# Performance work log

Hardware: AMD Instinct MI355X
Metric: run time of the kernel (lower is better)

## Reference

```python
import jax, jax.numpy as jnp
import numpy as np

B, L, H = 32, 2048, 512
EPS = 1e-6


def setup_inputs() -> dict:
    key = jax.random.key(0)
    k1, k2 = jax.random.split(key)
    hidden = jax.random.normal(k1, (B, L, H), dtype=jnp.float32)
    # nn.Linear(H, H): weight [H, H], bias [H]; use kaiming-uniform-like scale
    bound = 1.0 / np.sqrt(H)
    W = jax.random.uniform(k2, (H, H), dtype=jnp.float32, minval=-bound, maxval=bound)
    b = jnp.zeros((H,), dtype=jnp.float32)
    return {"hidden": hidden, "W": W, "b": b}


def reference(hidden, W, b):
    Bn, Ln, Hn = hidden.shape

    def step(M, k):
        # k: [B, H]; key == value == hidden[:, t, :]
        v_pred = jnp.einsum("bij,bj->bi", M, k)               # M @ k
        denom = jnp.sum(k * k, axis=-1, keepdims=True) + EPS   # [B, 1]
        delta_v = k - v_pred / denom                           # v - v_pred/denom (v == k)
        M = M + jnp.einsum("bi,bj->bij", delta_v, k)           # outer-product update
        return M, None

    M0 = jnp.zeros((Bn, Hn, Hn), dtype=hidden.dtype)
    xs = jnp.swapaxes(hidden[:, :-1, :], 0, 1)  # [L-1, B, H]
    M, _ = jax.lax.scan(step, M0, xs)

    query = hidden[:, -1, :]                                   # [B, H]
    context = jnp.einsum("bij,bj->bi", M, query)               # [B, H]
    return context @ W.T + b                                   # read_proj
```

## Files before the change

kernel.cpp:

```cpp
#include <hip/hip_runtime.h>
#include <hip/hip_fp16.h>

#define B_  32
#define L_  2048
#define H_  512
#define CA  64
#define NC  32
#define EPSF 1e-6f

typedef _Float16 f16x8 __attribute__((ext_vector_type(8)));
typedef float f32x16 __attribute__((ext_vector_type(16)));

template <int CTRL>
__device__ __forceinline__ float dpp_shift_add(float x) {
  int t = __builtin_amdgcn_update_dpp(0, __float_as_int(x), CTRL, 0xf, 0xf, true);
  return x + __int_as_float(t);
}
__device__ __forceinline__ float wave_reduce_lane63(float x) {
  x = dpp_shift_add<0x111>(x);
  x = dpp_shift_add<0x112>(x);
  x = dpp_shift_add<0x114>(x);
  x = dpp_shift_add<0x118>(x);
  x = dpp_shift_add<0x142>(x);
  x = dpp_shift_add<0x143>(x);
  return x;
}
__device__ __forceinline__ float rdlane(float v, int l) {
  return __int_as_float(__builtin_amdgcn_readlane(__float_as_int(v), l));
}
__device__ __forceinline__ void load_lds16h(const unsigned short* g, unsigned short* l) {
  __builtin_amdgcn_global_load_lds(
      (const __attribute__((address_space(1))) unsigned int*)(g),
      (__attribute__((address_space(3))) unsigned int*)(l), 16, 0, 0);
}

__global__ __launch_bounds__(256) void
deltarule_gram64(const float* __restrict__ hidden,
                 unsigned short* __restrict__ Kh,
                 float* __restrict__ tmT, float* __restrict__ dvec) {
  const int cb = blockIdx.x, b = blockIdx.y;
  const int tid = threadIdx.x, lane = tid & 63, wv = tid >> 6;
  __shared__ __align__(16) unsigned short Kf[CA * H_];
  __shared__ __align__(16) float G[CA * CA];

  const int c0 = cb * CA;
  const float* src = hidden + ((size_t)b * L_ + c0) * H_;
  unsigned short* kout = Kh + ((size_t)b * L_ + c0) * H_;
  const bool lastc = (cb == NC - 1);

#pragma unroll
  for (int u = 0; u < 16; ++u) {
    const int f8 = u * 256 + tid;
    const int row = f8 >> 6;
    const int colf = (f8 & 63) * 8;
    float4 va = *(const float4*)(src + row * H_ + colf);
    float4 vb = *(const float4*)(src + row * H_ + colf + 4);
    if (lastc && row == CA - 1) {
      va = make_float4(0.f, 0.f, 0.f, 0.f);
      vb = make_float4(0.f, 0.f, 0.f, 0.f);
    }
    __half2 h0 = __floats2half2_rn(va.x, va.y);
    __half2 h1 = __floats2half2_rn(va.z, va.w);
    __half2 h2 = __floats2half2_rn(vb.x, vb.y);
    __half2 h3 = __floats2half2_rn(vb.z, vb.w);
    uint4 pk = make_uint4(*(unsigned int*)&h0, *(unsigned int*)&h1,
                          *(unsigned int*)&h2, *(unsigned int*)&h3);
    *(uint4*)&Kf[((colf >> 3) * CA + row) * 8] = pk;
    *(uint4*)(kout + row * H_ + colf) = pk;
  }
  __syncthreads();

  if (wv < 3) {
    const int ta = (wv == 2) ? 1 : 0;
    const int tb = (wv == 0) ? 0 : 1;
    const int mrow = 32 * ta + (lane & 31);
    const int nrow = 32 * tb + (lane & 31);
    const int khi = lane >> 5;
    f32x16 acc;
#pragma unroll
    for (int r = 0; r < 16; ++r) acc[r] = 0.f;
#pragma unroll
    for (int kk = 0; kk < 32; ++kk) {
      const int k8 = 2 * kk + khi;
      const f16x8 av = *(const f16x8*)&Kf[(k8 * CA + mrow) * 8];
      const f16x8 bv = *(const f16x8*)&Kf[(k8 * CA + nrow) * 8];
      acc = __builtin_amdgcn_mfma_f32_32x32x16_f16(av, bv, acc, 0, 0, 0);
    }
#pragma unroll
    for (int r = 0; r < 16; ++r) {
      const int row32 = (r & 3) + 8 * (r >> 2) + 4 * khi;
      G[(32 * ta + row32) * CA + 32 * tb + (lane & 31)] = acc[r];
    }
  }
  __syncthreads();

  if (tid < CA) dvec[((size_t)b * NC + cb) * CA + tid] = G[tid * CA + tid] + EPSF;
  __syncthreads();

  if (wv == 0) {
    const int j = lane & 31;
    float X[32];
#pragma unroll
    for (int t = 31; t >= 0; --t) {
      float i0 = 0.f, i1 = 0.f;
#pragma unroll
      for (int s = t + 1; s < 32; s += 2) i0 = fmaf(G[t * CA + s], X[s], i0);
#pragma unroll
      for (int s = t + 2; s < 32; s += 2) i1 = fmaf(G[t * CA + s], X[s], i1);
      X[t] = (((j == t) ? 1.f : 0.f) - (i0 + i1)) / (G[t * CA + t] + EPSF);
    }
    if (lane < 32) {
#pragma unroll
      for (int t = 0; t < 32; ++t) G[t * CA + j] = X[t];
    }
  } else if (wv == 1) {
    const int j = lane & 31;
    float X[32];
#pragma unroll
    for (int t = 31; t >= 0; --t) {
      float i0 = 0.f, i1 = 0.f;
#pragma unroll
      for (int s = t + 1; s < 32; s += 2) i0 = fmaf(G[(32 + t) * CA + 32 + s], X[s], i0);
#pragma unroll
      for (int s = t + 2; s < 32; s += 2) i1 = fmaf(G[(32 + t) * CA + 32 + s], X[s], i1);
      X[t] = (((j == t) ? 1.f : 0.f) - (i0 + i1)) / (G[(32 + t) * CA + 32 + t] + EPSF);
    }
    if (lane < 32) {
#pragma unroll
      for (int t = 0; t < 32; ++t) G[(32 + t) * CA + 32 + j] = X[t];
    }
  }
  __syncthreads();

  const int zr = tid >> 3;
  const int zc = (tid & 7) * 4;
  float4 zf = make_float4(0.f, 0.f, 0.f, 0.f);
#pragma unroll
  for (int s = 0; s < 32; ++s) {
    const float u = G[zr * CA + 32 + s];
    const float4 xv = *(const float4*)&G[(32 + s) * CA + 32 + zc];
    zf.x = fmaf(u, xv.x, zf.x); zf.y = fmaf(u, xv.y, zf.y);
    zf.z = fmaf(u, xv.z, zf.z); zf.w = fmaf(u, xv.w, zf.w);
  }
  __syncthreads();
  *(float4*)&G[zr * CA + 32 + zc] = zf;
  __syncthreads();
  float4 yf = make_float4(0.f, 0.f, 0.f, 0.f);
#pragma unroll
  for (int s = 0; s < 32; ++s) {
    const float u = G[zr * CA + s];
    const float4 zv = *(const float4*)&G[s * CA + 32 + zc];
    yf.x = fmaf(u, zv.x, yf.x); yf.y = fmaf(u, zv.y, yf.y);
    yf.z = fmaf(u, zv.z, yf.z); yf.w = fmaf(u, zv.w, yf.w);
  }
  __syncthreads();
  *(float4*)&G[zr * CA + 32 + zc] = make_float4(-yf.x, -yf.y, -yf.z, -yf.w);
  __syncthreads();

  float* tout = tmT + ((size_t)b * NC + cb) * (CA * CA);
#pragma unroll
  for (int v = 0; v < 4; ++v) {
    const int f4 = v * 256 + tid;
    const int s = f4 >> 4;
    const int j4 = (f4 & 15) * 4;
    float4 val;
    if (s >= 32 && j4 < 32) val = make_float4(0.f, 0.f, 0.f, 0.f);
    else                    val = *(const float4*)&G[s * CA + j4];
    *(float4*)(tout + s * CA + j4) = val;
  }
}

__global__ __launch_bounds__(1024) void
deltarule_scan64w(const float* __restrict__ hidden,
                  const unsigned short* __restrict__ Kh,
                  const float* __restrict__ Wm, const float* __restrict__ bias,
                  const float* __restrict__ tmT, const float* __restrict__ dvec,
                  float* __restrict__ out) {
  const int b = blockIdx.x, tid = threadIdx.x, lane = tid & 63, wv = tid >> 6;
  __shared__ __align__(16) unsigned short KT[2][CA * H_];
  __shared__ __align__(16) float Part[16 * 64];
  __shared__ __align__(16) float Wv[H_];
  __shared__ __align__(16) float Ctx[H_];

  const unsigned short* khb = Kh + (size_t)b * L_ * H_;
  const float* tmb = tmT + (size_t)b * NC * (CA * CA);
  const float* dvb = dvec + (size_t)b * NC * CA;

  const int hh = tid & (H_ - 1);
  const bool wgroup = (tid < H_);
  float wh = 0.f, ch = 0.f;
  if (wgroup) {
    wh = hidden[((size_t)b * L_ + (L_ - 1)) * H_ + tid];
    Wv[tid] = wh;
  }

  {
    const unsigned short* s0 = khb + (size_t)(NC - 1) * CA * H_;
#pragma unroll
    for (int u = 0; u < 4; ++u) {
      const int off = (u * 16 + wv) * 512;
      load_lds16h(s0 + off + 8 * lane, &KT[(NC - 1) & 1][off]);
    }
  }
  float4 tA; float dCur;
  {
    tA = *(const float4*)(tmb + (size_t)(NC - 1) * (CA * CA) + lane * CA + 4 * wv);
    dCur = dvb[(NC - 1) * CA + lane];
  }
  asm volatile("s_waitcnt vmcnt(0) lgkmcnt(0)\n\ts_barrier" ::: "memory");

  for (int c = NC - 1; c >= 0; --c) {
    const int buf = c & 1;

    float4 nA; float dN = 0.f;
    if (c > 0) {
      nA = *(const float4*)(tmb + (size_t)(c - 1) * (CA * CA) + lane * CA + 4 * wv);
      dN = dvb[(c - 1) * CA + lane];
      const unsigned short* s1 = khb + (size_t)(c - 1) * CA * H_;
#pragma unroll
      for (int u = 0; u < 4; ++u) {
        const int off = (u * 16 + wv) * 512;
        load_lds16h(s1 + off + 8 * lane, &KT[buf ^ 1][off]);
      }
    }
    asm volatile("" ::: "memory");

    const float4 wa  = *(const float4*)&Wv[8 * lane];
    const float4 wb2 = *(const float4*)&Wv[8 * lane + 4];
    float ysg[4];
#pragma unroll
    for (int i = 0; i < 4; ++i) {
      const uint4 kr = *(const uint4*)&KT[buf][(4 * wv + i) * H_ + 8 * lane];
      const __half* kh = (const __half*)&kr;
      float p =            __half2float(kh[0]) * wa.x;
      p = fmaf(__half2float(kh[1]), wa.y, p);
      p = fmaf(__half2float(kh[2]), wa.z, p);
      p = fmaf(__half2float(kh[3]), wa.w, p);
      p = fmaf(__half2float(kh[4]), wb2.x, p);
      p = fmaf(__half2float(kh[5]), wb2.y, p);
      p = fmaf(__half2float(kh[6]), wb2.z, p);
      p = fmaf(__half2float(kh[7]), wb2.w, p);
      p = wave_reduce_lane63(p);
      ysg[i] = rdlane(p, 63);
    }

    float sp = ysg[0] * tA.x;
    sp = fmaf(ysg[1], tA.y, sp);
    sp = fmaf(ysg[2], tA.z, sp);
    sp = fmaf(ysg[3], tA.w, sp);
    Part[wv * 64 + lane] = sp;
    asm volatile("s_waitcnt lgkmcnt(0)\n\ts_barrier" ::: "memory");

    float sig = Part[lane];
#pragma unroll
    for (int w2 = 1; w2 < 16; ++w2) sig += Part[w2 * 64 + lane];
    const float src = wgroup ? sig : dCur * sig;

    const unsigned short* kcol = &KT[buf][0] + hh;
    float a0 = 0.f, a1 = 0.f, a2 = 0.f, a3 = 0.f;
#pragma unroll
    for (int t = 0; t < CA; t += 4) {
      a0 = fmaf(rdlane(src, t + 0), __half2float(*(const __half*)&kcol[(t + 0) * H_]), a0);
      a1 = fmaf(rdlane(src, t + 1), __half2float(*(const __half*)&kcol[(t + 1) * H_]), a1);
      a2 = fmaf(rdlane(src, t + 2), __half2float(*(const __half*)&kcol[(t + 2) * H_]), a2);
      a3 = fmaf(rdlane(src, t + 3), __half2float(*(const __half*)&kcol[(t + 3) * H_]), a3);
    }
    const float upd = (a0 + a1) + (a2 + a3);
    if (wgroup) { wh -= upd; Wv[tid] = wh; }
    else        { ch += upd; }

    if (c > 0) { dCur = dN; tA = nA; }
    asm volatile("s_waitcnt vmcnt(0) lgkmcnt(0)\n\ts_barrier" ::: "memory");
  }

  if (!wgroup) Ctx[hh] = ch;
  __syncthreads();
  {
    const int o = hh, hf = tid >> 9;
    float acc = 0.f;
    const float* wr = Wm + (size_t)o * H_ + hf * 256;
    const float* cx = &Ctx[hf * 256];
#pragma unroll 8
    for (int i = 0; i < 256; i += 4) {
      const float4 w4 = *(const float4*)(wr + i);
      const float4 cv = *(const float4*)(cx + i);
      acc = fmaf(w4.x, cv.x, acc); acc = fmaf(w4.y, cv.y, acc);
      acc = fmaf(w4.z, cv.z, acc); acc = fmaf(w4.w, cv.w, acc);
    }
    Part[hf * 512 + o] = acc;
  }
  __syncthreads();
  if (wgroup) out[(size_t)b * H_ + tid] = Part[tid] + Part[512 + tid] + bias[tid];
}

extern "C" void kernel_launch(void* const* d_in, const int* in_sizes, int n_in,
                              void* d_out, int out_size, void* d_ws, size_t ws_size,
                              hipStream_t stream) {
  (void)in_sizes; (void)n_in; (void)out_size; (void)ws_size;
  const float* hidden = (const float*)d_in[0];
  const float* Wm     = (const float*)d_in[1];
  const float* bias   = (const float*)d_in[2];
  float* out = (float*)d_out;

  const size_t szKh = (size_t)B_ * L_ * H_ * sizeof(unsigned short);
  unsigned short* Kh = (unsigned short*)d_ws;
  float* tmT  = (float*)((char*)d_ws + szKh);
  float* dvec = tmT + (size_t)B_ * NC * CA * CA;

  deltarule_gram64<<<dim3(NC, B_), 256, 0, stream>>>(hidden, Kh, tmT, dvec);
  deltarule_scan64w<<<B_, 1024, 0, stream>>>(hidden, Kh, Wm, bias, tmT, dvec, out);
}
```

Baseline: 341.0 us.

## Keep K chunk in registers and accumulate W/C updates via LDS atomics

The scan kernel no longer stages each key chunk in a double-buffered LDS tile. Each wave now keeps its four key rows in registers, prefetched one chunk ahead. The rank-64 updates to the query-side vector and the context vector are applied as per-wave partial sums through LDS atomicAdd into swizzled arrays, instead of a column-wise read of the whole LDS tile. Partial-sum reduction uses a padded layout with a DPP row reduce, and the gram kernel gains an XOR-swizzled LDS layout plus a register/readlane triangular solve. This trades LDS bandwidth and tile occupancy for LDS atomic contention and a change in summation order.

```diff
diff --git a/kernel.cpp b/kernel.cpp
--- a/kernel.cpp
+++ b/kernel.cpp
@@ -25,14 +25,18 @@
   x = dpp_shift_add<0x143>(x);
   return x;
 }
+__device__ __forceinline__ float row16_reduce(float x) {
+  x = dpp_shift_add<0x111>(x);
+  x = dpp_shift_add<0x112>(x);
+  x = dpp_shift_add<0x114>(x);
+  x = dpp_shift_add<0x118>(x);
+  return x;
+}
 __device__ __forceinline__ float rdlane(float v, int l) {
   return __int_as_float(__builtin_amdgcn_readlane(__float_as_int(v), l));
 }
-__device__ __forceinline__ void load_lds16h(const unsigned short* g, unsigned short* l) {
-  __builtin_amdgcn_global_load_lds(
-      (const __attribute__((address_space(1))) unsigned int*)(g),
-      (__attribute__((address_space(3))) unsigned int*)(l), 16, 0, 0);
-}
+
+#define KFI(row, k8) (((((row) * 64) + (k8)) * 8) ^ (((row) & 7) << 3))
 
 __global__ __launch_bounds__(256) void
 deltarule_gram64(const float* __restrict__ hidden,
@@ -65,7 +69,7 @@
     __half2 h3 = __floats2half2_rn(vb.z, vb.w);
     uint4 pk = make_uint4(*(unsigned int*)&h0, *(unsigned int*)&h1,
                           *(unsigned int*)&h2, *(unsigned int*)&h3);
-    *(uint4*)&Kf[((colf >> 3) * CA + row) * 8] = pk;
+    *(uint4*)&Kf[KFI(row, colf >> 3)] = pk;
     *(uint4*)(kout + row * H_ + colf) = pk;
   }
   __syncthreads();
@@ -82,8 +86,8 @@
 #pragma unroll
     for (int kk = 0; kk < 32; ++kk) {
       const int k8 = 2 * kk + khi;
-      const f16x8 av = *(const f16x8*)&Kf[(k8 * CA + mrow) * 8];
-      const f16x8 bv = *(const f16x8*)&Kf[(k8 * CA + nrow) * 8];
+      const f16x8 av = *(const f16x8*)&Kf[KFI(mrow, k8)];
+      const f16x8 bv = *(const f16x8*)&Kf[KFI(nrow, k8)];
       acc = __builtin_amdgcn_mfma_f32_32x32x16_f16(av, bv, acc, 0, 0, 0);
     }
 #pragma unroll
@@ -97,37 +101,24 @@
   if (tid < CA) dvec[((size_t)b * NC + cb) * CA + tid] = G[tid * CA + tid] + EPSF;
   __syncthreads();
 
-  if (wv == 0) {
+  if (wv < 2) {
+    const int off = wv * 32;
     const int j = lane & 31;
-    float X[32];
+    float Gr[32], X[32];
+#pragma unroll
+    for (int t = 0; t < 32; ++t) Gr[t] = G[(off + t) * CA + off + j];
 #pragma unroll
     for (int t = 31; t >= 0; --t) {
       float i0 = 0.f, i1 = 0.f;
 #pragma unroll
-      for (int s = t + 1; s < 32; s += 2) i0 = fmaf(G[t * CA + s], X[s], i0);
-#pragma unroll
-      for (int s = t + 2; s < 32; s += 2) i1 = fmaf(G[t * CA + s], X[s], i1);
-      X[t] = (((j == t) ? 1.f : 0.f) - (i0 + i1)) / (G[t * CA + t] + EPSF);
+      for (int s = t + 1; s < 32; s += 2) i0 = fmaf(rdlane(Gr[t], s), X[s], i0);
+#pragma unroll
+      for (int s = t + 2; s < 32; s += 2) i1 = fmaf(rdlane(Gr[t], s), X[s], i1);
+      X[t] = (((j == t) ? 1.f : 0.f) - (i0 + i1)) / (rdlane(Gr[t], t) + EPSF);
     }
     if (lane < 32) {
 #pragma unroll
-      for (int t = 0; t < 32; ++t) G[t * CA + j] = X[t];
-    }
-  } else if (wv == 1) {
-    const int j = lane & 31;
-    float X[32];
-#pragma unroll
-    for (int t = 31; t >= 0; --t) {
-      float i0 = 0.f, i1 = 0.f;
-#pragma unroll
-      for (int s = t + 1; s < 32; s += 2) i0 = fmaf(G[(32 + t) * CA + 32 + s], X[s], i0);
-#pragma unroll
-      for (int s = t + 2; s < 32; s += 2) i1 = fmaf(G[(32 + t) * CA + 32 + s], X[s], i1);
-      X[t] = (((j == t) ? 1.f : 0.f) - (i0 + i1)) / (G[(32 + t) * CA + 32 + t] + EPSF);
-    }
-    if (lane < 32) {
-#pragma unroll
-      for (int t = 0; t < 32; ++t) G[(32 + t) * CA + 32 + j] = X[t];
+      for (int t = 0; t < 32; ++t) G[(off + t) * CA + off + j] = X[t];
     }
   }
   __syncthreads();
@@ -171,75 +162,65 @@
 }
 
 __global__ __launch_bounds__(1024) void
-deltarule_scan64w(const float* __restrict__ hidden,
+deltarule_scan64r(const float* __restrict__ hidden,
                   const unsigned short* __restrict__ Kh,
                   const float* __restrict__ Wm, const float* __restrict__ bias,
                   const float* __restrict__ tmT, const float* __restrict__ dvec,
                   float* __restrict__ out) {
   const int b = blockIdx.x, tid = threadIdx.x, lane = tid & 63, wv = tid >> 6;
-  __shared__ __align__(16) unsigned short KT[2][CA * H_];
-  __shared__ __align__(16) float Part[16 * 64];
-  __shared__ __align__(16) float Wv[H_];
-  __shared__ __align__(16) float Ctx[H_];
+  __shared__ __align__(16) float Wsw[H_];
+  __shared__ __align__(16) float Csw[H_];
+  __shared__ __align__(16) float Part[64 * 17];
 
   const unsigned short* khb = Kh + (size_t)b * L_ * H_;
   const float* tmb = tmT + (size_t)b * NC * (CA * CA);
   const float* dvb = dvec + (size_t)b * NC * CA;
 
-  const int hh = tid & (H_ - 1);
-  const bool wgroup = (tid < H_);
-  float wh = 0.f, ch = 0.f;
-  if (wgroup) {
-    wh = hidden[((size_t)b * L_ + (L_ - 1)) * H_ + tid];
-    Wv[tid] = wh;
-  }
-
-  {
-    const unsigned short* s0 = khb + (size_t)(NC - 1) * CA * H_;
-#pragma unroll
-    for (int u = 0; u < 4; ++u) {
-      const int off = (u * 16 + wv) * 512;
-      load_lds16h(s0 + off + 8 * lane, &KT[(NC - 1) & 1][off]);
-    }
-  }
-  float4 tA; float dCur;
-  {
-    tA = *(const float4*)(tmb + (size_t)(NC - 1) * (CA * CA) + lane * CA + 4 * wv);
-    dCur = dvb[(NC - 1) * CA + lane];
-  }
+  if (tid < H_) {
+    const float q = hidden[((size_t)b * L_ + (L_ - 1)) * H_ + tid];
+    const int p = ((tid & 4) << 6) + ((tid >> 3) << 2) + (tid & 3);
+    Wsw[p] = q;
+    Csw[p] = 0.f;
+  }
+
+  uint4 kr[4];
+  float4 tA;
+  float dv;
+#pragma unroll
+  for (int i = 0; i < 4; ++i)
+    kr[i] = *(const uint4*)(khb + ((size_t)(NC - 1) * CA + 4 * wv + i) * H_ + 8 * lane);
+  tA = *(const float4*)(tmb + (size_t)(NC - 1) * (CA * CA) + lane * CA + 4 * wv);
+  dv = dvb[(NC - 1) * CA + lane];
   asm volatile("s_waitcnt vmcnt(0) lgkmcnt(0)\n\ts_barrier" ::: "memory");
 
   for (int c = NC - 1; c >= 0; --c) {
-    const int buf = c & 1;
-
-    float4 nA; float dN = 0.f;
+    uint4 kn[4];
+    float4 nA;
+    float dN = 0.f;
     if (c > 0) {
+#pragma unroll
+      for (int i = 0; i < 4; ++i)
+        kn[i] = *(const uint4*)(khb + ((size_t)(c - 1) * CA + 4 * wv + i) * H_ + 8 * lane);
       nA = *(const float4*)(tmb + (size_t)(c - 1) * (CA * CA) + lane * CA + 4 * wv);
       dN = dvb[(c - 1) * CA + lane];
-      const unsigned short* s1 = khb + (size_t)(c - 1) * CA * H_;
-#pragma unroll
-      for (int u = 0; u < 4; ++u) {
-        const int off = (u * 16 + wv) * 512;
-        load_lds16h(s1 + off + 8 * lane, &KT[buf ^ 1][off]);
-      }
-    }
-    asm volatile("" ::: "memory");
-
-    const float4 wa  = *(const float4*)&Wv[8 * lane];
-    const float4 wb2 = *(const float4*)&Wv[8 * lane + 4];
+    }
+
+    const float4 wa  = *(const float4*)&Wsw[4 * lane];
+    const float4 wb2 = *(const float4*)&Wsw[256 + 4 * lane];
+    float kf[4][8];
     float ysg[4];
 #pragma unroll
     for (int i = 0; i < 4; ++i) {
-      const uint4 kr = *(const uint4*)&KT[buf][(4 * wv + i) * H_ + 8 * lane];
-      const __half* kh = (const __half*)&kr;
-      float p =            __half2float(kh[0]) * wa.x;
-      p = fmaf(__half2float(kh[1]), wa.y, p);
-      p = fmaf(__half2float(kh[2]), wa.z, p);
-      p = fmaf(__half2float(kh[3]), wa.w, p);
-      p = fmaf(__half2float(kh[4]), wb2.x, p);
-      p = fmaf(__half2float(kh[5]), wb2.y, p);
-      p = fmaf(__half2float(kh[6]), wb2.z, p);
-      p = fmaf(__half2float(kh[7]), wb2.w, p);
+      const float2 f0 = __half22float2(*(const __half2*)&kr[i].x);
+      const float2 f1 = __half22float2(*(const __half2*)&kr[i].y);
+      const float2 f2 = __half22float2(*(const __half2*)&kr[i].z);
+      const float2 f3 = __half22float2(*(const __half2*)&kr[i].w);
+      kf[i][0] = f0.x; kf[i][1] = f0.y; kf[i][2] = f1.x; kf[i][3] = f1.y;
+      kf[i][4] = f2.x; kf[i][5] = f2.y; kf[i][6] = f3.x; kf[i][7] = f3.y;
+      float p = f0.x * wa.x;
+      p = fmaf(f0.y, wa.y, p); p = fmaf(f1.x, wa.z, p); p = fmaf(f1.y, wa.w, p);
+      p = fmaf(f2.x, wb2.x, p); p = fmaf(f2.y, wb2.y, p);
+      p = fmaf(f3.x, wb2.z, p); p = fmaf(f3.y, wb2.w, p);
       p = wave_reduce_lane63(p);
       ysg[i] = rdlane(p, 63);
     }
@@ -248,49 +229,72 @@
     sp = fmaf(ysg[1], tA.y, sp);
     sp = fmaf(ysg[2], tA.z, sp);
     sp = fmaf(ysg[3], tA.w, sp);
-    Part[wv * 64 + lane] = sp;
+    Part[lane * 17 + wv] = sp;
     asm volatile("s_waitcnt lgkmcnt(0)\n\ts_barrier" ::: "memory");
 
-    float sig = Part[lane];
-#pragma unroll
-    for (int w2 = 1; w2 < 16; ++w2) sig += Part[w2 * 64 + lane];
-    const float src = wgroup ? sig : dCur * sig;
-
-    const unsigned short* kcol = &KT[buf][0] + hh;
-    float a0 = 0.f, a1 = 0.f, a2 = 0.f, a3 = 0.f;
-#pragma unroll
-    for (int t = 0; t < CA; t += 4) {
-      a0 = fmaf(rdlane(src, t + 0), __half2float(*(const __half*)&kcol[(t + 0) * H_]), a0);
-      a1 = fmaf(rdlane(src, t + 1), __half2float(*(const __half*)&kcol[(t + 1) * H_]), a1);
-      a2 = fmaf(rdlane(src, t + 2), __half2float(*(const __half*)&kcol[(t + 2) * H_]), a2);
-      a3 = fmaf(rdlane(src, t + 3), __half2float(*(const __half*)&kcol[(t + 3) * H_]), a3);
-    }
-    const float upd = (a0 + a1) + (a2 + a3);
-    if (wgroup) { wh -= upd; Wv[tid] = wh; }
-    else        { ch += upd; }
-
-    if (c > 0) { dCur = dN; tA = nA; }
+    float red = Part[(4 * wv + (lane >> 4)) * 17 + (lane & 15)];
+    red = row16_reduce(red);
+    const float sg0 = rdlane(red, 15);
+    const float sg1 = rdlane(red, 31);
+    const float sg2 = rdlane(red, 47);
+    const float sg3 = rdlane(red, 63);
+    const float sv0 = sg0 * rdlane(dv, 4 * wv + 0);
+    const float sv1 = sg1 * rdlane(dv, 4 * wv + 1);
+    const float sv2 = sg2 * rdlane(dv, 4 * wv + 2);
+    const float sv3 = sg3 * rdlane(dv, 4 * wv + 3);
+
+    float wsum[8], csum[8];
+#pragma unroll
+    for (int e = 0; e < 8; ++e) {
+      float ws = sg0 * kf[0][e];
+      ws = fmaf(sg1, kf[1][e], ws);
+      ws = fmaf(sg2, kf[2][e], ws);
+      ws = fmaf(sg3, kf[3][e], ws);
+      float cs = sv0 * kf[0][e];
+      cs = fmaf(sv1, kf[1][e], cs);
+      cs = fmaf(sv2, kf[2][e], cs);
+      cs = fmaf(sv3, kf[3][e], cs);
+      wsum[e] = ws; csum[e] = cs;
+    }
+    const int g = (lane >> 3) & 3;
+#pragma unroll
+    for (int r = 0; r < 4; ++r) {
+      const int k = (r + g) & 3;
+      const bool s1 = (k & 2) != 0, s0 = (k & 1) != 0;
+      const float wl  = s1 ? (s0 ? wsum[3] : wsum[2]) : (s0 ? wsum[1] : wsum[0]);
+      const float whh = s1 ? (s0 ? wsum[7] : wsum[6]) : (s0 ? wsum[5] : wsum[4]);
+      const float cl  = s1 ? (s0 ? csum[3] : csum[2]) : (s0 ? csum[1] : csum[0]);
+      const float chh = s1 ? (s0 ? csum[7] : csum[6]) : (s0 ? csum[5] : csum[4]);
+      atomicAdd(&Wsw[4 * lane + k], -wl);
+      atomicAdd(&Csw[4 * lane + k],  cl);
+      atomicAdd(&Wsw[256 + 4 * lane + k], -whh);
+      atomicAdd(&Csw[256 + 4 * lane + k],  chh);
+    }
+
+    if (c > 0) {
+      dv = dN; tA = nA;
+#pragma unroll
+      for (int i = 0; i < 4; ++i) kr[i] = kn[i];
+    }
     asm volatile("s_waitcnt vmcnt(0) lgkmcnt(0)\n\ts_barrier" ::: "memory");
   }
 
-  if (!wgroup) Ctx[hh] = ch;
-  __syncthreads();
   {
-    const int o = hh, hf = tid >> 9;
+    const int o = tid & (H_ - 1);
+    const int hf = tid >> 9;
     float acc = 0.f;
     const float* wr = Wm + (size_t)o * H_ + hf * 256;
-    const float* cx = &Ctx[hf * 256];
 #pragma unroll 8
     for (int i = 0; i < 256; i += 4) {
       const float4 w4 = *(const float4*)(wr + i);
-      const float4 cv = *(const float4*)(cx + i);
+      const float4 cv = *(const float4*)&Csw[((i & 4) << 6) + hf * 128 + ((i >> 3) << 2)];
       acc = fmaf(w4.x, cv.x, acc); acc = fmaf(w4.y, cv.y, acc);
       acc = fmaf(w4.z, cv.z, acc); acc = fmaf(w4.w, cv.w, acc);
     }
     Part[hf * 512 + o] = acc;
   }
   __syncthreads();
-  if (wgroup) out[(size_t)b * H_ + tid] = Part[tid] + Part[512 + tid] + bias[tid];
+  if (tid < H_) out[(size_t)b * H_ + tid] = Part[tid] + Part[512 + tid] + bias[tid];
 }
 
 extern "C" void kernel_launch(void* const* d_in, const int* in_sizes, int n_in,
@@ -308,5 +312,5 @@
   float* dvec = tmT + (size_t)B_ * NC * CA * CA;
 
   deltarule_gram64<<<dim3(NC, B_), 256, 0, stream>>>(hidden, Kh, tmT, dvec);
-  deltarule_scan64w<<<B_, 1024, 0, stream>>>(hidden, Kh, Wm, bias, tmT, dvec, out);
-}
+  deltarule_scan64r<<<B_, 1024, 0, stream>>>(hidden, Kh, Wm, bias, tmT, dvec, out);
+}
```

New measurement: 963.1 us. 182% more time.
